# Kernel optimization log

Measured on AMD Instinct MI355X. Metric: run time of the kernel, lower is better.

Reference implementation:

```python
import jax, jax.numpy as jnp
import numpy as np

BATCH = 1024
A = 128  # image height
B = 128  # image width (must equal A for the original matmul chain to type-check)
N = 64   # attention grid size
H = 1024 # h_dim


def setup_inputs() -> dict:
    key = jax.random.key(0)
    k0, k1, k2, k3 = jax.random.split(key, 4)
    x = jax.random.normal(k0, (BATCH, A * B), dtype=jnp.float32)
    x_hat = jax.random.normal(k1, (BATCH, A * B), dtype=jnp.float32)
    h = jax.random.normal(k2, (BATCH, H), dtype=jnp.float32)
    W_read_w = jax.random.normal(k3, (5, H), dtype=jnp.float32) * 0.02
    W_read_b = jnp.zeros((5,), dtype=jnp.float32)
    return {"x": x, "x_hat": x_hat, "h": h, "W_read_w": W_read_w, "W_read_b": W_read_b}


def _compute_filterbanks(params):
    # params: (5,) from W_read(h)[0]
    gt_X, gt_Y, log_var, log_dt = params[0], params[1], params[2], params[3]
    var = jnp.exp(log_var + 1e-8)
    # .item() in the original detaches these from the autograd graph
    g_X = jax.lax.stop_gradient((A + 1) * (gt_X + 1) / 2)
    g_Y = jax.lax.stop_gradient((B + 1) * (gt_Y + 1) / 2)
    d = jax.lax.stop_gradient(jnp.exp(log_dt) * (max(A, B) - 1) / (N - 1))
    # linspace(g + (-N/2-0.5)d, g + (N-1-N/2-0.5)d, N) == g + (i - N/2 - 0.5)*d
    idx = jnp.arange(N, dtype=jnp.float32) - N / 2 - 0.5  # (N,)
    mu_X = g_X + idx * d  # (N,)
    mu_Y = g_Y + idx * d  # (N,)
    a = jnp.arange(A, dtype=jnp.float32)
    b = jnp.arange(B, dtype=jnp.float32)
    F_X = jnp.exp(-((a[None, :] - mu_X[:, None]) ** 2) / (2 * var))  # (N, A)
    F_Y = jnp.exp(-((b[None, :] - mu_Y[:, None]) ** 2) / (2 * var))  # (N, B)
    # NOTE: original normalizes by the GLOBAL sum, not per-row
    F_X = F_X / jnp.sum(F_X)
    F_Y = F_Y / jnp.sum(F_Y)
    return F_X, F_Y


def reference(x, x_hat, h, W_read_w, W_read_b):
    # params from FIRST batch element, shared across the whole batch (as in original)
    params = (h @ W_read_w.T + W_read_b)[0]  # (5,)
    gamma = jnp.exp(params[4])
    F_X, F_Y = _compute_filterbanks(params)  # (N,A), (N,B)

    xi = x.reshape(-1, A, B)
    xh = x_hat.reshape(-1, A, B)

    def filt(z):  # gamma * F_Y @ z @ F_X.T  -> (batch, N, N)
        t = jnp.einsum('na,kab->knb', F_Y, z)      # (batch, N, B)
        return gamma * jnp.einsum('knb,mb->knm', t, F_X)

    x_filt = filt(xi).reshape(-1, N * N)
    x_hat_filt = filt(xh).reshape(-1, N * N)
    return jnp.concatenate([x_filt, x_hat_filt], axis=1)  # (batch, 2*N*N)
```

## Files before the change

### kernel.cpp

```cpp
#include <hip/hip_runtime.h>
#include <math.h>

#define AB 128
#define NN 64
#define HD 1024

#define SFZ 256.0f
#define SFF 64.0f
#define DESCALE (1.0f / 1048576.0f)

typedef _Float16 half8 __attribute__((ext_vector_type(8)));
typedef float f32x4 __attribute__((ext_vector_type(4)));
typedef unsigned u32x4 __attribute__((ext_vector_type(4)));


__device__ __forceinline__ float wave_reduce(float v) {
  v += __shfl_down(v, 32);
  v += __shfl_down(v, 16);
  v += __shfl_down(v, 8);
  v += __shfl_down(v, 4);
  v += __shfl_down(v, 2);
  v += __shfl_down(v, 1);
  return v;
}

__global__ __launch_bounds__(1024) void fb_setup(
    const float* __restrict__ h, const float* __restrict__ Ww,
    const float* __restrict__ Wb, void* __restrict__ wsv) {
  __shared__ float redp[16][5];
  __shared__ float reds[16][2];
  __shared__ float sc[5];
  __shared__ float ssum[2];
  const int tid = threadIdx.x;
  const int lane = tid & 63;
  const int wv = tid >> 6;

  const float hv = h[tid];
  float p[5];
#pragma unroll
  for (int j = 0; j < 5; ++j) p[j] = hv * Ww[j * HD + tid];
#pragma unroll
  for (int j = 0; j < 5; ++j) {
    float r = wave_reduce(p[j]);
    if (lane == 0) redp[wv][j] = r;
  }
  __syncthreads();
  if (tid < 5) {
    float s = Wb[tid];
#pragma unroll
    for (int w = 0; w < 16; ++w) s += redp[w][tid];
    sc[tid] = s;
  }
  __syncthreads();

  const float gt_X = sc[0], gt_Y = sc[1], log_var = sc[2], log_dt = sc[3];
  const float var = expf(log_var + 1e-8f);
  const float g_X = (129.0f * (gt_X + 1.0f)) / 2.0f;
  const float g_Y = (129.0f * (gt_Y + 1.0f)) / 2.0f;
  const float d = (expf(log_dt) * 127.0f) / 63.0f;
  const float twovar = 2.0f * var;

  float fyv[8], fxv[8];
  float sY = 0.f, sX = 0.f;
#pragma unroll
  for (int c = 0; c < 8; ++c) {
    const int idx = tid + 1024 * c;
    const int n = idx >> 7;
    const int col = idx & 127;
    const float idxn = (float)n - 32.5f;
    const float muX = g_X + idxn * d;
    const float muY = g_Y + idxn * d;
    const float dx = (float)col - muX;
    const float dy = (float)col - muY;
    const float fx = expf(-(dx * dx) / twovar);
    const float fy = expf(-(dy * dy) / twovar);
    fyv[c] = fy;
    fxv[c] = fx;
    sY += fy;
    sX += fx;
  }
  {
    float rY = wave_reduce(sY);
    float rX = wave_reduce(sX);
    if (lane == 0) { reds[wv][0] = rY; reds[wv][1] = rX; }
  }
  __syncthreads();
  if (tid < 2) {
    float s = 0.f;
#pragma unroll
    for (int w = 0; w < 16; ++w) s += reds[w][tid];
    ssum[tid] = s;
  }
  __syncthreads();
  const float invY = 1.0f / ssum[0];
  const float invX = 1.0f / ssum[1];

  _Float16* FXk = (_Float16*)wsv;
  _Float16* FYhi = (_Float16*)wsv + 2 * NN * AB;
  _Float16* FYlo = FYhi + NN * AB;

#pragma unroll
  for (int c = 0; c < 8; ++c) {
    const int idx = tid + 1024 * c;
    const int n = idx >> 7;
    const int col = idx & 127;
    const float vy = fyv[c] * invY * SFF;
    const float vx = fxv[c] * invX * SFF;
    const _Float16 yh = (_Float16)vy;
    const _Float16 xh2 = (_Float16)vx;
    FYhi[idx] = yh;
    FYlo[idx] = (_Float16)(vy - (float)yh);
    const int kaddr = ((col >> 3) << 9) + (n << 3) + (col & 7);
    FXk[kaddr] = xh2;
    FXk[8192 + kaddr] = (_Float16)(vx - (float)xh2);
  }
  if (tid == 0) ((float*)wsv)[16384] = expf(sc[4]) * DESCALE;
}

__device__ __forceinline__ void split8(const f32x4 z0, const f32x4 z1,
                                       float s, half8& hi, half8& lo) {
#pragma unroll
  for (int e = 0; e < 8; ++e) {
    const float q = (e < 4 ? z0[e] : z1[e - 4]) * s;
    const _Float16 hh = (_Float16)q;
    hi[e] = hh;
    lo[e] = (_Float16)(q - (float)hh);
  }
}

__global__ __launch_bounds__(256, 5) void fb_filt(
    const float* __restrict__ x, const float* __restrict__ xh,
    const void* __restrict__ wsv, float* __restrict__ out) {
  __shared__ __align__(16) _Float16 S_lds[2 * NN * AB];

  const int tid = threadIdx.x;
  const int lane = tid & 63;
  const int wv = tid >> 6;
  const int l15 = lane & 15;
  const int h4 = lane >> 4;
  const int bid = blockIdx.x;
  const int img = bid >> 1;
  const int which = bid & 1;
  const float* __restrict__ Z = (which ? xh : x) + (size_t)img * (AB * AB);
  const _Float16* __restrict__ FYhi = (const _Float16*)wsv + 2 * NN * AB;
  const _Float16* __restrict__ FYlo = FYhi + NN * AB;
  const float gamma_eff = ((const float*)wsv)[16384];

  const float* __restrict__ zrow = Z + (32 * wv + l15) * AB + 8 * h4;
  f32x4 z[4][4];
#pragma unroll
  for (int ks = 0; ks < 2; ++ks) {
    const float* p0 = zrow + 32 * ks;
    const float* p1 = zrow + 16 * AB + 32 * ks;
    z[ks][0] = *(const f32x4*)p0;
    z[ks][1] = *(const f32x4*)(p0 + 4);
    z[ks][2] = *(const f32x4*)p1;
    z[ks][3] = *(const f32x4*)(p1 + 4);
  }
  {
    const u32x4* __restrict__ src = (const u32x4*)wsv;
    u32x4* __restrict__ dst = (u32x4*)S_lds;
#pragma unroll
    for (int c = 0; c < 8; ++c) dst[c * 256 + tid] = src[c * 256 + tid];
  }
  __syncthreads();

#pragma unroll
  for (int ks = 2; ks < 4; ++ks) {
    const float* p0 = zrow + 32 * ks;
    const float* p1 = zrow + 16 * AB + 32 * ks;
    z[ks][0] = *(const f32x4*)p0;
    z[ks][1] = *(const f32x4*)(p0 + 4);
    z[ks][2] = *(const f32x4*)p1;
    z[ks][3] = *(const f32x4*)(p1 + 4);
  }
  __builtin_amdgcn_sched_barrier(0);

  f32x4 acc[4][2];
#pragma unroll
  for (int mt = 0; mt < 4; ++mt)
#pragma unroll
    for (int j = 0; j < 2; ++j) acc[mt][j] = {0.f, 0.f, 0.f, 0.f};

#pragma unroll
  for (int ks = 0; ks < 4; ++ks) {
    half8 bhi[2], blo[2];
    split8(z[ks][0], z[ks][1], SFZ, bhi[0], blo[0]);
    split8(z[ks][2], z[ks][3], SFZ, bhi[1], blo[1]);
    const int gbase = ((4 * ks + h4) << 9);
#pragma unroll
    for (int mt = 0; mt < 4; ++mt) {
      const _Float16* ap = S_lds + gbase + ((16 * mt + l15) << 3);
      const half8 ahi = *(const half8*)ap;
      const half8 alo = *(const half8*)(ap + 8192);
#pragma unroll
      for (int j = 0; j < 2; ++j) {
        acc[mt][j] = __builtin_amdgcn_mfma_f32_16x16x32_f16(ahi, bhi[j], acc[mt][j], 0, 0, 0);
        acc[mt][j] = __builtin_amdgcn_mfma_f32_16x16x32_f16(ahi, blo[j], acc[mt][j], 0, 0, 0);
        acc[mt][j] = __builtin_amdgcn_mfma_f32_16x16x32_f16(alo, bhi[j], acc[mt][j], 0, 0, 0);
      }
    }
  }
  __syncthreads();

#pragma unroll
  for (int mt = 0; mt < 4; ++mt) {
#pragma unroll
    for (int j = 0; j < 2; ++j) {
      const int abase = ((4 * wv + 2 * j + (l15 >> 3)) << 9) + (l15 & 7);
#pragma unroll
      for (int r = 0; r < 4; ++r) {
        const int row = 16 * mt + 4 * h4 + r;
        const float v = acc[mt][j][r];
        const _Float16 hh = (_Float16)v;
        const _Float16 ll = (_Float16)(v - (float)hh);
        S_lds[abase + (row << 3)] = hh;
        S_lds[8192 + abase + (row << 3)] = ll;
      }
    }
  }

  half8 fyh[4], fyl[4];
#pragma unroll
  for (int ks = 0; ks < 4; ++ks) {
    const int foff = (16 * wv + l15) * AB + 32 * ks + 8 * h4;
    fyh[ks] = *(const half8*)(FYhi + foff);
    fyl[ks] = *(const half8*)(FYlo + foff);
  }
  __builtin_amdgcn_sched_barrier(0);
  __syncthreads();

  f32x4 acc2[4];
#pragma unroll
  for (int mt = 0; mt < 4; ++mt) acc2[mt] = {0.f, 0.f, 0.f, 0.f};

#pragma unroll
  for (int ks = 0; ks < 4; ++ks) {
    const int gbase = ((4 * ks + h4) << 9);
#pragma unroll
    for (int mt = 0; mt < 4; ++mt) {
      const _Float16* bp = S_lds + gbase + ((16 * mt + l15) << 3);
      const half8 bh = *(const half8*)bp;
      const half8 bl = *(const half8*)(bp + 8192);
      acc2[mt] = __builtin_amdgcn_mfma_f32_16x16x32_f16(fyh[ks], bh, acc2[mt], 0, 0, 0);
      acc2[mt] = __builtin_amdgcn_mfma_f32_16x16x32_f16(fyh[ks], bl, acc2[mt], 0, 0, 0);
      acc2[mt] = __builtin_amdgcn_mfma_f32_16x16x32_f16(fyl[ks], bh, acc2[mt], 0, 0, 0);
    }
  }

  float* __restrict__ ob = out + (size_t)img * 8192 + which * 4096;
#pragma unroll
  for (int mt = 0; mt < 4; ++mt) {
#pragma unroll
    for (int r = 0; r < 4; ++r) {
      ob[(16 * wv + 4 * h4 + r) * 64 + 16 * mt + l15] = acc2[mt][r] * gamma_eff;
    }
  }
}

extern "C" void kernel_launch(void* const* d_in, const int* in_sizes, int n_in,
                              void* d_out, int out_size, void* d_ws, size_t ws_size,
                              hipStream_t stream) {
  const float* x = (const float*)d_in[0];
  const float* xh = (const float*)d_in[1];
  const float* h = (const float*)d_in[2];
  const float* Ww = (const float*)d_in[3];
  const float* Wb = (const float*)d_in[4];
  float* outp = (float*)d_out;

  fb_setup<<<1, 1024, 0, stream>>>(h, Ww, Wb, d_ws);
  fb_filt<<<2048, 256, 0, stream>>>(x, xh, (const void*)d_ws, outp);
}
```

Baseline: 183.3 us.

## Issue image loads via inline asm with staged vmcnt waits per k-step

Replaces the compiler-scheduled image loads with 16 inline-asm dwordx4 loads, all issued after the LDS filter copy. Each first-stage k-step now waits only for its own slice, using s_waitcnt vmcnt(12/8/4/0), so MFMA work starts before the whole tile has arrived. The FY filter loads are hoisted to before the LDS restaging, and the launch-bounds occupancy hint drops from 5 to 4 to give the extra live registers room. The trade-off is that none of the image loads now start before the LDS-copy barrier, where half of them used to. The lower occupancy also means less latency hiding across waves.

After: 178.8 us. 1.03x faster.

```diff
diff --git a/kernel.cpp b/kernel.cpp
--- a/kernel.cpp
+++ b/kernel.cpp
@@ -128,7 +128,17 @@
   }
 }
 
-__global__ __launch_bounds__(256, 5) void fb_filt(
+#define ZLD(dst, base, OFF)                                              \
+  asm volatile("global_load_dwordx4 %0, %1, off offset:" #OFF            \
+               : "=v"(dst) : "v"(base))
+
+#define WAITVM_SB(N)                                                     \
+  do {                                                                   \
+    asm volatile("s_waitcnt vmcnt(" #N ")");                             \
+    __builtin_amdgcn_sched_barrier(0);                                   \
+  } while (0)
+
+__global__ __launch_bounds__(256, 4) void fb_filt(
     const float* __restrict__ x, const float* __restrict__ xh,
     const void* __restrict__ wsv, float* __restrict__ out) {
   __shared__ __align__(16) _Float16 S_lds[2 * NN * AB];
@@ -146,17 +156,6 @@
   const _Float16* __restrict__ FYlo = FYhi + NN * AB;
   const float gamma_eff = ((const float*)wsv)[16384];
 
-  const float* __restrict__ zrow = Z + (32 * wv + l15) * AB + 8 * h4;
-  f32x4 z[4][4];
-#pragma unroll
-  for (int ks = 0; ks < 2; ++ks) {
-    const float* p0 = zrow + 32 * ks;
-    const float* p1 = zrow + 16 * AB + 32 * ks;
-    z[ks][0] = *(const f32x4*)p0;
-    z[ks][1] = *(const f32x4*)(p0 + 4);
-    z[ks][2] = *(const f32x4*)p1;
-    z[ks][3] = *(const f32x4*)(p1 + 4);
-  }
   {
     const u32x4* __restrict__ src = (const u32x4*)wsv;
     u32x4* __restrict__ dst = (u32x4*)S_lds;
@@ -165,16 +164,18 @@
   }
   __syncthreads();
 
-#pragma unroll
-  for (int ks = 2; ks < 4; ++ks) {
-    const float* p0 = zrow + 32 * ks;
-    const float* p1 = zrow + 16 * AB + 32 * ks;
-    z[ks][0] = *(const f32x4*)p0;
-    z[ks][1] = *(const f32x4*)(p0 + 4);
-    z[ks][2] = *(const f32x4*)p1;
-    z[ks][3] = *(const f32x4*)(p1 + 4);
-  }
-  __builtin_amdgcn_sched_barrier(0);
+  const float* zb0 = Z + (32 * wv + l15) * AB + 8 * h4;
+  const float* zb1 = zb0 + 16 * AB;
+  f32x4 z0_0, z0_1, z0_2, z0_3, z1_0, z1_1, z1_2, z1_3;
+  f32x4 z2_0, z2_1, z2_2, z2_3, z3_0, z3_1, z3_2, z3_3;
+  ZLD(z0_0, zb0, 0);   ZLD(z0_1, zb0, 16);
+  ZLD(z0_2, zb1, 0);   ZLD(z0_3, zb1, 16);
+  ZLD(z1_0, zb0, 128); ZLD(z1_1, zb0, 144);
+  ZLD(z1_2, zb1, 128); ZLD(z1_3, zb1, 144);
+  ZLD(z2_0, zb0, 256); ZLD(z2_1, zb0, 272);
+  ZLD(z2_2, zb1, 256); ZLD(z2_3, zb1, 272);
+  ZLD(z3_0, zb0, 384); ZLD(z3_1, zb0, 400);
+  ZLD(z3_2, zb1, 384); ZLD(z3_3, zb1, 400);
 
   f32x4 acc[4][2];
 #pragma unroll
@@ -182,26 +183,42 @@
 #pragma unroll
     for (int j = 0; j < 2; ++j) acc[mt][j] = {0.f, 0.f, 0.f, 0.f};
 
+#define S1_KS(KS, WN)                                                          \
+  do {                                                                         \
+    WAITVM_SB(WN);                                                             \
+    half8 bhi0, blo0, bhi1, blo1;                                              \
+    split8(z##KS##_0, z##KS##_1, SFZ, bhi0, blo0);                             \
+    split8(z##KS##_2, z##KS##_3, SFZ, bhi1, blo1);                             \
+    const int gbase = ((4 * (KS) + h4) << 9);                                  \
+    _Pragma("unroll")                                                          \
+    for (int mt = 0; mt < 4; ++mt) {                                           \
+      const _Float16* ap = S_lds + gbase + ((16 * mt + l15) << 3);             \
+      const half8 ahi = *(const half8*)ap;                                     \
+      const half8 alo = *(const half8*)(ap + 8192);                            \
+      acc[mt][0] = __builtin_amdgcn_mfma_f32_16x16x32_f16(ahi, bhi0, acc[mt][0], 0, 0, 0); \
+      acc[mt][0] = __builtin_amdgcn_mfma_f32_16x16x32_f16(ahi, blo0, acc[mt][0], 0, 0, 0); \
+      acc[mt][0] = __builtin_amdgcn_mfma_f32_16x16x32_f16(alo, bhi0, acc[mt][0], 0, 0, 0); \
+      acc[mt][1] = __builtin_amdgcn_mfma_f32_16x16x32_f16(ahi, bhi1, acc[mt][1], 0, 0, 0); \
+      acc[mt][1] = __builtin_amdgcn_mfma_f32_16x16x32_f16(ahi, blo1, acc[mt][1], 0, 0, 0); \
+      acc[mt][1] = __builtin_amdgcn_mfma_f32_16x16x32_f16(alo, bhi1, acc[mt][1], 0, 0, 0); \
+    }                                                                          \
+  } while (0)
+
+  S1_KS(0, 12);
+  S1_KS(1, 8);
+  S1_KS(2, 4);
+  S1_KS(3, 0);
+#undef S1_KS
+
+  __syncthreads();
+
+  half8 fyh[4], fyl[4];
 #pragma unroll
   for (int ks = 0; ks < 4; ++ks) {
-    half8 bhi[2], blo[2];
-    split8(z[ks][0], z[ks][1], SFZ, bhi[0], blo[0]);
-    split8(z[ks][2], z[ks][3], SFZ, bhi[1], blo[1]);
-    const int gbase = ((4 * ks + h4) << 9);
-#pragma unroll
-    for (int mt = 0; mt < 4; ++mt) {
-      const _Float16* ap = S_lds + gbase + ((16 * mt + l15) << 3);
-      const half8 ahi = *(const half8*)ap;
-      const half8 alo = *(const half8*)(ap + 8192);
-#pragma unroll
-      for (int j = 0; j < 2; ++j) {
-        acc[mt][j] = __builtin_amdgcn_mfma_f32_16x16x32_f16(ahi, bhi[j], acc[mt][j], 0, 0, 0);
-        acc[mt][j] = __builtin_amdgcn_mfma_f32_16x16x32_f16(ahi, blo[j], acc[mt][j], 0, 0, 0);
-        acc[mt][j] = __builtin_amdgcn_mfma_f32_16x16x32_f16(alo, bhi[j], acc[mt][j], 0, 0, 0);
-      }
-    }
-  }
-  __syncthreads();
+    const int foff = (16 * wv + l15) * AB + 32 * ks + 8 * h4;
+    fyh[ks] = *(const half8*)(FYhi + foff);
+    fyl[ks] = *(const half8*)(FYlo + foff);
+  }
 
 #pragma unroll
   for (int mt = 0; mt < 4; ++mt) {
@@ -219,15 +236,6 @@
       }
     }
   }
-
-  half8 fyh[4], fyl[4];
-#pragma unroll
-  for (int ks = 0; ks < 4; ++ks) {
-    const int foff = (16 * wv + l15) * AB + 32 * ks + 8 * h4;
-    fyh[ks] = *(const half8*)(FYhi + foff);
-    fyl[ks] = *(const half8*)(FYlo + foff);
-  }
-  __builtin_amdgcn_sched_barrier(0);
   __syncthreads();
 
   f32x4 acc2[4];
```
